# Kernel optimization log

Measured on AMD Instinct MI355X. Metric: run time of the kernel, lower is better.

## Reference

```python
import jax, jax.numpy as jnp
import numpy as np

D_MODEL, D_K, H = 1024, 64, 16
B, S = 2, 2048

def setup_inputs() -> dict:
    key = jax.random.key(0)
    ks = jax.random.split(key, 9)
    s_in = 1.0 / np.sqrt(D_MODEL)
    x = jax.random.normal(ks[0], (B, S, D_MODEL), dtype=jnp.float32)
    Wq = jax.random.uniform(ks[1], (H, D_MODEL, D_K), jnp.float32, -s_in, s_in)
    bq = jax.random.uniform(ks[2], (H, D_K), jnp.float32, -s_in, s_in)
    Wk = jax.random.uniform(ks[3], (H, D_MODEL, D_K), jnp.float32, -s_in, s_in)
    bk = jax.random.uniform(ks[4], (H, D_K), jnp.float32, -s_in, s_in)
    Wv = jax.random.uniform(ks[5], (H, D_MODEL, D_K), jnp.float32, -s_in, s_in)
    bv = jax.random.uniform(ks[6], (H, D_K), jnp.float32, -s_in, s_in)
    Wo = jax.random.uniform(ks[7], (D_MODEL, D_MODEL), jnp.float32, -s_in, s_in)
    bo = jax.random.uniform(ks[8], (D_MODEL,), jnp.float32, -s_in, s_in)
    return {"x": x, "Wq": Wq, "bq": bq, "Wk": Wk, "bk": bk,
            "Wv": Wv, "bv": bv, "Wo": Wo, "bo": bo}

def reference(x, Wq, bq, Wk, bk, Wv, bv, Wo, bo):
    # PositionLinear = Linear + ReLU (the ReLU is part of the original math)
    Q = jax.nn.relu(jnp.einsum('bsd,hdk->bhsk', x, Wq) + bq[:, None, :])
    K = jax.nn.relu(jnp.einsum('bsd,hdk->bhsk', x, Wk) + bk[:, None, :])
    V = jax.nn.relu(jnp.einsum('bsd,hdk->bhsk', x, Wv) + bv[:, None, :])
    scale = jnp.sqrt(jnp.float32(Q.shape[-1]))
    scores = jnp.einsum('bhsk,bhtk->bhst', Q, K) / scale  # [B,H,S,S]
    attn = jax.nn.softmax(scores, axis=-1)
    ctx = jnp.einsum('bhst,bhtk->bhsk', attn, V)
    # concat heads along feature dim (head order matches torch.cat(output, 2))
    ctx = jnp.transpose(ctx, (0, 2, 1, 3)).reshape(x.shape[0], x.shape[1], -1)
    out = jax.nn.relu(ctx @ Wo + bo)
    return out
```

## Files before the change

### kernel.cpp

```cpp
#include <hip/hip_runtime.h>
#include <cstddef>

#define D_MODEL 1024
#define DK 64
#define NH 16
#define NB 2
#define SEQ 2048

typedef __attribute__((ext_vector_type(8))) short bf16x8;
typedef __attribute__((ext_vector_type(4))) float floatx4;

static __device__ __forceinline__ unsigned short f2bf(float f) {
    union { float f; unsigned u; } v; v.f = f;
    unsigned r = (v.u + 0x7fffu + ((v.u >> 16) & 1u)) >> 16;
    return (unsigned short)r;
}

static __device__ __forceinline__ unsigned pk2bf(float lo, float hi) {
    unsigned ua = __float_as_uint(lo) + 0x8000u;
    unsigned ub = __float_as_uint(hi) + 0x8000u;
    return __builtin_amdgcn_perm(ub, ua, 0x07060302u);
}

static __device__ __forceinline__ float swz16(float x) {
    return __int_as_float(__builtin_amdgcn_ds_swizzle(__float_as_int(x), 0x401F));
}

static __device__ __forceinline__ void gld16(const unsigned short* g, unsigned short* l) {
    __builtin_amdgcn_global_load_lds(
        (const __attribute__((address_space(1))) unsigned int*)g,
        (__attribute__((address_space(3))) unsigned int*)l, 16, 0, 0);
}

__global__ __launch_bounds__(256) void convert_x(const float* __restrict__ x,
                                                 unsigned short* __restrict__ xb)
{
    const size_t i = ((size_t)blockIdx.x * 256 + threadIdx.x) * 16;
#pragma unroll
    for (int c = 0; c < 16; c += 4) {
        float4 v = *(const float4*)&x[i + c];
        uint2 pk;
        pk.x = (unsigned)f2bf(v.x) | ((unsigned)f2bf(v.y) << 16);
        pk.y = (unsigned)f2bf(v.z) | ((unsigned)f2bf(v.w) << 16);
        *(uint2*)&xb[i + c] = pk;
    }
}

__global__ __launch_bounds__(256) void pack_w(
    const float* __restrict__ Wq, const float* __restrict__ Wk,
    const float* __restrict__ Wv, const float* __restrict__ Wo,
    unsigned short* __restrict__ Bqkv, unsigned short* __restrict__ Bo)
{
    __shared__ float T[64][65];
    const int t   = blockIdx.x;
    const int tid = threadIdx.x;
    const int rr   = tid >> 2;
    const int cseg = (tid & 3) * 16;

    const float* src;
    unsigned short* dst;
    if (t < 768) {
        const int proj = t / 256, rem = t % 256;
        const int h = rem >> 4, d0 = (rem & 15) * 64;
        const float* W = proj == 0 ? Wq : (proj == 1 ? Wk : Wv);
        src = W + ((size_t)h * 1024 + d0) * 64;
#pragma unroll
        for (int c = 0; c < 16; c += 4) {
            float4 v = *(const float4*)&src[(size_t)rr * 64 + cseg + c];
            T[rr][cseg + c + 0] = v.x; T[rr][cseg + c + 1] = v.y;
            T[rr][cseg + c + 2] = v.z; T[rr][cseg + c + 3] = v.w;
        }
        __syncthreads();
        dst = &Bqkv[((size_t)proj * 1024 + h * 64 + rr) * 1024 + d0 + cseg];
    } else {
        const int t2 = t - 768;
        const int k0 = (t2 >> 4) * 64, nb0 = (t2 & 15) * 64;
#pragma unroll
        for (int c = 0; c < 16; c += 4) {
            float4 v = *(const float4*)&Wo[(size_t)(k0 + rr) * 1024 + nb0 + cseg + c];
            T[rr][cseg + c + 0] = v.x; T[rr][cseg + c + 1] = v.y;
            T[rr][cseg + c + 2] = v.z; T[rr][cseg + c + 3] = v.w;
        }
        __syncthreads();
        dst = &Bo[(size_t)(nb0 + rr) * 1024 + k0 + cseg];
    }
    unsigned int w[8];
#pragma unroll
    for (int ii = 0; ii < 8; ii++) {
        unsigned short lo = f2bf(T[cseg + ii * 2 + 0][rr]);
        unsigned short hi = f2bf(T[cseg + ii * 2 + 1][rr]);
        w[ii] = (unsigned)lo | ((unsigned)hi << 16);
    }
    *(uint4*)(dst + 0) = make_uint4(w[0], w[1], w[2], w[3]);
    *(uint4*)(dst + 8) = make_uint4(w[4], w[5], w[6], w[7]);
}

__global__ __launch_bounds__(256) void gemm_qkv(
    const unsigned short* __restrict__ Abf,
    const unsigned short* __restrict__ Bp,
    const float* __restrict__ bq, const float* __restrict__ bk,
    const float* __restrict__ bv,
    unsigned short* __restrict__ Qo, unsigned short* __restrict__ Ko,
    unsigned short* __restrict__ Vo)
{
    __shared__ __align__(16) unsigned short As[128 * 32];
    __shared__ __align__(16) unsigned short Bs[128 * 32];

    const int tid  = threadIdx.x;
    const int wv   = tid >> 6, lane = tid & 63;
    const int m0   = blockIdx.x * 128;
    const int n0   = blockIdx.y * 128;
    const int lq   = lane & 15, g = lane >> 4;
    const int wm   = (wv >> 1) * 64;
    const int wn   = (wv & 1) * 64;
    const int srow = lane >> 2;
    const int sseg = (lane & 3) * 8;

    floatx4 acc[4][4];
#pragma unroll
    for (int i = 0; i < 4; i++)
#pragma unroll
        for (int j = 0; j < 4; j++) acc[i][j] = (floatx4){0.f, 0.f, 0.f, 0.f};

    for (int k0 = 0; k0 < 1024; k0 += 32) {
#pragma unroll
        for (int r = 0; r < 2; r++) {
            const int chunk = wv * 2 + r;
            const int row   = chunk * 16 + srow;
            gld16(&Abf[(size_t)(m0 + row) * 1024 + k0 + sseg], &As[chunk * 512]);
            gld16(&Bp [(size_t)(n0 + row) * 1024 + k0 + sseg], &Bs[chunk * 512]);
        }
        __syncthreads();
        bf16x8 af[4], bfv[4];
#pragma unroll
        for (int i = 0; i < 4; i++)
            af[i] = *(const bf16x8*)&As[(wm + i * 16 + lq) * 32 + g * 8];
#pragma unroll
        for (int j = 0; j < 4; j++)
            bfv[j] = *(const bf16x8*)&Bs[(wn + j * 16 + lq) * 32 + g * 8];
#pragma unroll
        for (int i = 0; i < 4; i++)
#pragma unroll
            for (int j = 0; j < 4; j++)
                acc[i][j] = __builtin_amdgcn_mfma_f32_16x16x32_bf16(af[i], bfv[j], acc[i][j], 0, 0, 0);
        __syncthreads();
    }

    const int proj = n0 >> 10;
    const float* bias = proj == 0 ? bq : (proj == 1 ? bk : bv);
    unsigned short* OutQK = proj == 0 ? Qo : Ko;

#pragma unroll
    for (int j = 0; j < 4; j++) {
        const int n  = n0 + wn + j * 16 + lq;
        const int nn = n & 1023;
        const int h  = nn >> 6, dk = nn & 63;
        const float bb = bias[nn];
#pragma unroll
        for (int i = 0; i < 4; i++) {
            const int mbase = m0 + wm + i * 16 + g * 4;
            const int b_ = mbase >> 11;
            const int s_ = mbase & (SEQ - 1);
            const int bh = b_ * NH + h;
            if (proj < 2) {
                const size_t fb = (((size_t)bh * 128 + (s_ >> 4)) * 2 + (dk >> 5)) * 512
                                + (size_t)((((dk & 31) >> 3) * 16) + (s_ & 15)) * 8 + (dk & 7);
#pragma unroll
                for (int r = 0; r < 4; r++)
                    OutQK[fb + (size_t)r * 8] = f2bf(fmaxf(acc[i][j][r] + bb, 0.f));
            } else {
                const size_t fb = ((((size_t)bh * 32 + (s_ >> 6)) * 4 + (dk >> 4)) * 2
                                   + ((s_ >> 5) & 1)) * 512
                                + (size_t)((((s_ & 31) >> 3) * 16) + (dk & 15)) * 8 + (s_ & 7);
                uint2 pk;
                pk.x = (unsigned)f2bf(fmaxf(acc[i][j][0] + bb, 0.f))
                     | ((unsigned)f2bf(fmaxf(acc[i][j][1] + bb, 0.f)) << 16);
                pk.y = (unsigned)f2bf(fmaxf(acc[i][j][2] + bb, 0.f))
                     | ((unsigned)f2bf(fmaxf(acc[i][j][3] + bb, 0.f)) << 16);
                *(uint2*)&Vo[fb] = pk;
            }
        }
    }
}

__global__ __launch_bounds__(256, 2) void attn_kernel(
    const unsigned short* __restrict__ Qf,
    const unsigned short* __restrict__ Kf,
    const unsigned short* __restrict__ Vf,
    unsigned short* __restrict__ ctxb)
{
    __shared__ __align__(16) unsigned short KVs[2][8192];
    __shared__ __align__(16) unsigned short Ps[4][2][16][72];

    const int blk = blockIdx.x;
    const int xcd = blk & 7;
    const int j_  = blk >> 3;
    const int bh  = xcd * 4 + (j_ & 3);
    const int qt  = j_ >> 2;

    const int tid  = threadIdx.x;
    const int wv   = tid >> 6;
    const int lane = tid & 63;
    const int lq   = lane & 15;
    const int g    = lane >> 4;

    const int q0 = qt * 128 + wv * 32;

    const size_t qfB = ((size_t)bh * 128 + (q0 >> 4)) * 1024 + (size_t)lane * 8;
    bf16x8 q0a = *(const bf16x8*)&Qf[qfB];
    bf16x8 q0b = *(const bf16x8*)&Qf[qfB + 512];
    bf16x8 q1a = *(const bf16x8*)&Qf[qfB + 1024];
    bf16x8 q1b = *(const bf16x8*)&Qf[qfB + 1536];

    const float C  = 0.18033688011112042f;
    const float MC = 2.8853900817779267f;

    const unsigned short* KtB = &Kf[(size_t)bh * 131072];
    const unsigned short* VtB = &Vf[(size_t)bh * 131072];

    float l0 = 0.f, l1 = 0.f;
    floatx4 acc0[4], acc1[4];
#pragma unroll
    for (int i = 0; i < 4; i++) {
        acc0[i] = (floatx4){0.f, 0.f, 0.f, 0.f};
        acc1[i] = (floatx4){0.f, 0.f, 0.f, 0.f};
    }

#pragma unroll
    for (int r = 0; r < 2; r++) {
        const int c = wv * 2 + r;
        gld16(&KtB[(size_t)c * 512 + lane * 8], &KVs[0][c * 512]);
        gld16(&VtB[(size_t)c * 512 + lane * 8], &KVs[0][4096 + c * 512]);
    }
    __syncthreads();

    for (int jt = 0; jt < SEQ / 64; jt++) {
        const int buf = jt & 1;

        const int jn = (jt + 1) & (SEQ / 64 - 1);
        const unsigned short* ktn = &KtB[(size_t)jn * 4096];
        const unsigned short* vtn = &VtB[(size_t)jn * 4096];
#pragma unroll
        for (int r = 0; r < 2; r++) {
            const int c = wv * 2 + r;
            gld16(&ktn[(size_t)c * 512 + lane * 8], &KVs[buf ^ 1][c * 512]);
            gld16(&vtn[(size_t)c * 512 + lane * 8], &KVs[buf ^ 1][4096 + c * 512]);
        }

        const unsigned short* kb = &KVs[buf][0];
        const unsigned short* vb = &KVs[buf][4096];

        floatx4 s0[4], s1[4];
#pragma unroll
        for (int mt = 0; mt < 4; mt++) {
            bf16x8 a0 = *(const bf16x8*)&kb[mt * 1024 + lane * 8];
            bf16x8 a1 = *(const bf16x8*)&kb[mt * 1024 + 512 + lane * 8];
            s0[mt] = (floatx4){0.f, 0.f, 0.f, 0.f};
            s0[mt] = __builtin_amdgcn_mfma_f32_16x16x32_bf16(a0, q0a, s0[mt], 0, 0, 0);
            s0[mt] = __builtin_amdgcn_mfma_f32_16x16x32_bf16(a1, q0b, s0[mt], 0, 0, 0);
            s1[mt] = (floatx4){0.f, 0.f, 0.f, 0.f};
            s1[mt] = __builtin_amdgcn_mfma_f32_16x16x32_bf16(a0, q1a, s1[mt], 0, 0, 0);
            s1[mt] = __builtin_amdgcn_mfma_f32_16x16x32_bf16(a1, q1b, s1[mt], 0, 0, 0);
        }

        bf16x8 vr[8];
#pragma unroll
        for (int nt = 0; nt < 4; nt++) {
            vr[nt]     = *(const bf16x8*)&vb[nt * 1024 + lane * 8];
            vr[4 + nt] = *(const bf16x8*)&vb[nt * 1024 + 512 + lane * 8];
        }

#pragma unroll
        for (int mt = 0; mt < 4; mt++) {
            float p00 = __builtin_amdgcn_exp2f(fmaf(s0[mt][0], C, -MC));
            float p01 = __builtin_amdgcn_exp2f(fmaf(s0[mt][1], C, -MC));
            float p02 = __builtin_amdgcn_exp2f(fmaf(s0[mt][2], C, -MC));
            float p03 = __builtin_amdgcn_exp2f(fmaf(s0[mt][3], C, -MC));
            l0 += (p00 + p01) + (p02 + p03);
            uint2 pk;
            pk.x = pk2bf(p00, p01);
            pk.y = pk2bf(p02, p03);
            *(uint2*)&Ps[wv][0][lq][mt * 16 + g * 4] = pk;
            float p10 = __builtin_amdgcn_exp2f(fmaf(s1[mt][0], C, -MC));
            float p11 = __builtin_amdgcn_exp2f(fmaf(s1[mt][1], C, -MC));
            float p12 = __builtin_amdgcn_exp2f(fmaf(s1[mt][2], C, -MC));
            float p13 = __builtin_amdgcn_exp2f(fmaf(s1[mt][3], C, -MC));
            l1 += (p10 + p11) + (p12 + p13);
            uint2 pk1;
            pk1.x = pk2bf(p10, p11);
            pk1.y = pk2bf(p12, p13);
            *(uint2*)&Ps[wv][1][lq][mt * 16 + g * 4] = pk1;
        }
        __builtin_amdgcn_s_waitcnt(0xC07F);
        bf16x8 pb00 = *(const bf16x8*)&Ps[wv][0][lq][g * 8];
        bf16x8 pb01 = *(const bf16x8*)&Ps[wv][0][lq][32 + g * 8];
        bf16x8 pb10 = *(const bf16x8*)&Ps[wv][1][lq][g * 8];
        bf16x8 pb11 = *(const bf16x8*)&Ps[wv][1][lq][32 + g * 8];

#pragma unroll
        for (int nt = 0; nt < 4; nt++) {
            acc0[nt] = __builtin_amdgcn_mfma_f32_16x16x32_bf16(vr[nt],     pb00, acc0[nt], 0, 0, 0);
            acc0[nt] = __builtin_amdgcn_mfma_f32_16x16x32_bf16(vr[4 + nt], pb01, acc0[nt], 0, 0, 0);
            acc1[nt] = __builtin_amdgcn_mfma_f32_16x16x32_bf16(vr[nt],     pb10, acc1[nt], 0, 0, 0);
            acc1[nt] = __builtin_amdgcn_mfma_f32_16x16x32_bf16(vr[4 + nt], pb11, acc1[nt], 0, 0, 0);
        }

        __syncthreads();
    }

    l0 += swz16(l0); l0 += __shfl_xor(l0, 32, 64);
    l1 += swz16(l1); l1 += __shfl_xor(l1, 32, 64);
    const float li0 = 1.f / l0, li1 = 1.f / l1;
    const int b_ = bh >> 4, h_ = bh & 15;
#pragma unroll
    for (int nt = 0; nt < 4; nt++) {
        uint2 pk;
        pk.x = pk2bf(acc0[nt][0] * li0, acc0[nt][1] * li0);
        pk.y = pk2bf(acc0[nt][2] * li0, acc0[nt][3] * li0);
        *(uint2*)&ctxb[((size_t)(b_ * SEQ) + q0 + lq) * D_MODEL + h_ * DK + nt * 16 + g * 4] = pk;
        uint2 pk1;
        pk1.x = pk2bf(acc1[nt][0] * li1, acc1[nt][1] * li1);
        pk1.y = pk2bf(acc1[nt][2] * li1, acc1[nt][3] * li1);
        *(uint2*)&ctxb[((size_t)(b_ * SEQ) + q0 + 16 + lq) * D_MODEL + h_ * DK + nt * 16 + g * 4] = pk1;
    }
}

__global__ __launch_bounds__(256) void gemm_o(
    const unsigned short* __restrict__ Abf,
    const unsigned short* __restrict__ Bp,
    const float* __restrict__ bo,
    float* __restrict__ out)
{
    __shared__ __align__(16) unsigned short As[128 * 32];
    __shared__ __align__(16) unsigned short Bs[128 * 32];

    const int tid  = threadIdx.x;
    const int wv   = tid >> 6, lane = tid & 63;
    const int m0   = blockIdx.x * 128;
    const int n0   = blockIdx.y * 128;
    const int lq   = lane & 15, g = lane >> 4;
    const int wm   = (wv >> 1) * 64;
    const int wn   = (wv & 1) * 64;
    const int srow = lane >> 2;
    const int sseg = (lane & 3) * 8;

    floatx4 acc[4][4];
#pragma unroll
    for (int i = 0; i < 4; i++)
#pragma unroll
        for (int j = 0; j < 4; j++) acc[i][j] = (floatx4){0.f, 0.f, 0.f, 0.f};

    for (int k0 = 0; k0 < 1024; k0 += 32) {
#pragma unroll
        for (int r = 0; r < 2; r++) {
            const int chunk = wv * 2 + r;
            const int row   = chunk * 16 + srow;
            gld16(&Abf[(size_t)(m0 + row) * 1024 + k0 + sseg], &As[chunk * 512]);
            gld16(&Bp [(size_t)(n0 + row) * 1024 + k0 + sseg], &Bs[chunk * 512]);
        }
        __syncthreads();
        bf16x8 af[4], bfv[4];
#pragma unroll
        for (int i = 0; i < 4; i++)
            af[i] = *(const bf16x8*)&As[(wm + i * 16 + lq) * 32 + g * 8];
#pragma unroll
        for (int j = 0; j < 4; j++)
            bfv[j] = *(const bf16x8*)&Bs[(wn + j * 16 + lq) * 32 + g * 8];
#pragma unroll
        for (int i = 0; i < 4; i++)
#pragma unroll
            for (int j = 0; j < 4; j++)
                acc[i][j] = __builtin_amdgcn_mfma_f32_16x16x32_bf16(af[i], bfv[j], acc[i][j], 0, 0, 0);
        __syncthreads();
    }

#pragma unroll
    for (int j = 0; j < 4; j++) {
        const int n  = n0 + wn + j * 16 + lq;
        const float bb = bo[n];
#pragma unroll
        for (int i = 0; i < 4; i++) {
#pragma unroll
            for (int r = 0; r < 4; r++) {
                const int m = m0 + wm + i * 16 + g * 4 + r;
                out[(size_t)m * 1024 + n] = fmaxf(acc[i][j][r] + bb, 0.f);
            }
        }
    }
}

extern "C" void kernel_launch(void* const* d_in, const int* in_sizes, int n_in,
                              void* d_out, int out_size, void* d_ws, size_t ws_size,
                              hipStream_t stream) {
    const float* x  = (const float*)d_in[0];
    const float* Wq = (const float*)d_in[1];
    const float* bq = (const float*)d_in[2];
    const float* Wk = (const float*)d_in[3];
    const float* bk = (const float*)d_in[4];
    const float* Wv = (const float*)d_in[5];
    const float* bv = (const float*)d_in[6];
    const float* Wo = (const float*)d_in[7];
    const float* bo = (const float*)d_in[8];
    float* out = (float*)d_out;

    const size_t perE = (size_t)NB * NH * SEQ * DK;
    unsigned short* xbf  = (unsigned short*)d_ws;
    unsigned short* Bqkv = xbf  + (size_t)4096 * 1024;
    unsigned short* Bo   = Bqkv + (size_t)3072 * 1024;
    unsigned short* Qfr  = Bo   + (size_t)1024 * 1024;
    unsigned short* Kfr  = Qfr + perE;
    unsigned short* Vfr  = Kfr + perE;
    unsigned short* Cbf  = Vfr + perE;

    convert_x<<<1024, 256, 0, stream>>>(x, xbf);
    pack_w<<<1024, 256, 0, stream>>>(Wq, Wk, Wv, Wo, Bqkv, Bo);
    gemm_qkv<<<dim3(32, 24), 256, 0, stream>>>(xbf, Bqkv, bq, bk, bv, Qfr, Kfr, Vfr);
    attn_kernel<<<512, 256, 0, stream>>>(Qfr, Kfr, Vfr, Cbf);
    gemm_o<<<dim3(32, 8), 256, 0, stream>>>(Cbf, Bo, bo, out);
}
```

Baseline: 196.4 us.

## Split attention work across waves by key halves with LDS reduction

```diff
diff --git a/kernel.cpp b/kernel.cpp
--- a/kernel.cpp
+++ b/kernel.cpp
@@ -190,7 +190,8 @@
     unsigned short* __restrict__ ctxb)
 {
     __shared__ __align__(16) unsigned short KVs[2][8192];
-    __shared__ __align__(16) unsigned short Ps[4][2][16][72];
+    __shared__ __align__(16) unsigned short Ps[4][4][16][40];
+    __shared__ float Lx[2][4][64];
 
     const int blk = blockIdx.x;
     const int xcd = blk & 7;
@@ -203,14 +204,18 @@
     const int lane = tid & 63;
     const int lq   = lane & 15;
     const int g    = lane >> 4;
-
-    const int q0 = qt * 128 + wv * 32;
-
+    const int qh   = wv >> 1;
+    const int kh   = wv & 1;
+
+    const int q0 = qt * 128 + qh * 64;
+
+    bf16x8 qa[4], qb[4];
     const size_t qfB = ((size_t)bh * 128 + (q0 >> 4)) * 1024 + (size_t)lane * 8;
-    bf16x8 q0a = *(const bf16x8*)&Qf[qfB];
-    bf16x8 q0b = *(const bf16x8*)&Qf[qfB + 512];
-    bf16x8 q1a = *(const bf16x8*)&Qf[qfB + 1024];
-    bf16x8 q1b = *(const bf16x8*)&Qf[qfB + 1536];
+#pragma unroll
+    for (int t = 0; t < 4; t++) {
+        qa[t] = *(const bf16x8*)&Qf[qfB + (size_t)t * 1024];
+        qb[t] = *(const bf16x8*)&Qf[qfB + (size_t)t * 1024 + 512];
+    }
 
     const float C  = 0.18033688011112042f;
     const float MC = 2.8853900817779267f;
@@ -218,13 +223,12 @@
     const unsigned short* KtB = &Kf[(size_t)bh * 131072];
     const unsigned short* VtB = &Vf[(size_t)bh * 131072];
 
-    float l0 = 0.f, l1 = 0.f;
-    floatx4 acc0[4], acc1[4];
-#pragma unroll
-    for (int i = 0; i < 4; i++) {
-        acc0[i] = (floatx4){0.f, 0.f, 0.f, 0.f};
-        acc1[i] = (floatx4){0.f, 0.f, 0.f, 0.f};
-    }
+    float l[4] = {0.f, 0.f, 0.f, 0.f};
+    floatx4 acc[4][4];
+#pragma unroll
+    for (int t = 0; t < 4; t++)
+#pragma unroll
+        for (int n = 0; n < 4; n++) acc[t][n] = (floatx4){0.f, 0.f, 0.f, 0.f};
 
 #pragma unroll
     for (int r = 0; r < 2; r++) {
@@ -250,78 +254,95 @@
         const unsigned short* kb = &KVs[buf][0];
         const unsigned short* vb = &KVs[buf][4096];
 
-        floatx4 s0[4], s1[4];
-#pragma unroll
-        for (int mt = 0; mt < 4; mt++) {
-            bf16x8 a0 = *(const bf16x8*)&kb[mt * 1024 + lane * 8];
-            bf16x8 a1 = *(const bf16x8*)&kb[mt * 1024 + 512 + lane * 8];
-            s0[mt] = (floatx4){0.f, 0.f, 0.f, 0.f};
-            s0[mt] = __builtin_amdgcn_mfma_f32_16x16x32_bf16(a0, q0a, s0[mt], 0, 0, 0);
-            s0[mt] = __builtin_amdgcn_mfma_f32_16x16x32_bf16(a1, q0b, s0[mt], 0, 0, 0);
-            s1[mt] = (floatx4){0.f, 0.f, 0.f, 0.f};
-            s1[mt] = __builtin_amdgcn_mfma_f32_16x16x32_bf16(a0, q1a, s1[mt], 0, 0, 0);
-            s1[mt] = __builtin_amdgcn_mfma_f32_16x16x32_bf16(a1, q1b, s1[mt], 0, 0, 0);
-        }
-
-        bf16x8 vr[8];
-#pragma unroll
-        for (int nt = 0; nt < 4; nt++) {
-            vr[nt]     = *(const bf16x8*)&vb[nt * 1024 + lane * 8];
-            vr[4 + nt] = *(const bf16x8*)&vb[nt * 1024 + 512 + lane * 8];
-        }
-
-#pragma unroll
-        for (int mt = 0; mt < 4; mt++) {
-            float p00 = __builtin_amdgcn_exp2f(fmaf(s0[mt][0], C, -MC));
-            float p01 = __builtin_amdgcn_exp2f(fmaf(s0[mt][1], C, -MC));
-            float p02 = __builtin_amdgcn_exp2f(fmaf(s0[mt][2], C, -MC));
-            float p03 = __builtin_amdgcn_exp2f(fmaf(s0[mt][3], C, -MC));
-            l0 += (p00 + p01) + (p02 + p03);
-            uint2 pk;
-            pk.x = pk2bf(p00, p01);
-            pk.y = pk2bf(p02, p03);
-            *(uint2*)&Ps[wv][0][lq][mt * 16 + g * 4] = pk;
-            float p10 = __builtin_amdgcn_exp2f(fmaf(s1[mt][0], C, -MC));
-            float p11 = __builtin_amdgcn_exp2f(fmaf(s1[mt][1], C, -MC));
-            float p12 = __builtin_amdgcn_exp2f(fmaf(s1[mt][2], C, -MC));
-            float p13 = __builtin_amdgcn_exp2f(fmaf(s1[mt][3], C, -MC));
-            l1 += (p10 + p11) + (p12 + p13);
+        bf16x8 k0a = *(const bf16x8*)&kb[(2 * kh + 0) * 1024 + lane * 8];
+        bf16x8 k0b = *(const bf16x8*)&kb[(2 * kh + 0) * 1024 + 512 + lane * 8];
+        bf16x8 k1a = *(const bf16x8*)&kb[(2 * kh + 1) * 1024 + lane * 8];
+        bf16x8 k1b = *(const bf16x8*)&kb[(2 * kh + 1) * 1024 + 512 + lane * 8];
+
+        bf16x8 vr[4];
+#pragma unroll
+        for (int n = 0; n < 4; n++)
+            vr[n] = *(const bf16x8*)&vb[(n * 2 + kh) * 512 + lane * 8];
+
+#pragma unroll
+        for (int t = 0; t < 4; t++) {
+            floatx4 s0 = (floatx4){0.f, 0.f, 0.f, 0.f};
+            s0 = __builtin_amdgcn_mfma_f32_16x16x32_bf16(k0a, qa[t], s0, 0, 0, 0);
+            s0 = __builtin_amdgcn_mfma_f32_16x16x32_bf16(k0b, qb[t], s0, 0, 0, 0);
+            floatx4 s1 = (floatx4){0.f, 0.f, 0.f, 0.f};
+            s1 = __builtin_amdgcn_mfma_f32_16x16x32_bf16(k1a, qa[t], s1, 0, 0, 0);
+            s1 = __builtin_amdgcn_mfma_f32_16x16x32_bf16(k1b, qb[t], s1, 0, 0, 0);
+
+            float p00 = __builtin_amdgcn_exp2f(fmaf(s0[0], C, -MC));
+            float p01 = __builtin_amdgcn_exp2f(fmaf(s0[1], C, -MC));
+            float p02 = __builtin_amdgcn_exp2f(fmaf(s0[2], C, -MC));
+            float p03 = __builtin_amdgcn_exp2f(fmaf(s0[3], C, -MC));
+            l[t] += (p00 + p01) + (p02 + p03);
+            uint2 pk0;
+            pk0.x = pk2bf(p00, p01);
+            pk0.y = pk2bf(p02, p03);
+            *(uint2*)&Ps[wv][t][lq][g * 4] = pk0;
+
+            float p10 = __builtin_amdgcn_exp2f(fmaf(s1[0], C, -MC));
+            float p11 = __builtin_amdgcn_exp2f(fmaf(s1[1], C, -MC));
+            float p12 = __builtin_amdgcn_exp2f(fmaf(s1[2], C, -MC));
+            float p13 = __builtin_amdgcn_exp2f(fmaf(s1[3], C, -MC));
+            l[t] += (p10 + p11) + (p12 + p13);
             uint2 pk1;
             pk1.x = pk2bf(p10, p11);
             pk1.y = pk2bf(p12, p13);
-            *(uint2*)&Ps[wv][1][lq][mt * 16 + g * 4] = pk1;
+            *(uint2*)&Ps[wv][t][lq][16 + g * 4] = pk1;
         }
         __builtin_amdgcn_s_waitcnt(0xC07F);
-        bf16x8 pb00 = *(const bf16x8*)&Ps[wv][0][lq][g * 8];
-        bf16x8 pb01 = *(const bf16x8*)&Ps[wv][0][lq][32 + g * 8];
-        bf16x8 pb10 = *(const bf16x8*)&Ps[wv][1][lq][g * 8];
-        bf16x8 pb11 = *(const bf16x8*)&Ps[wv][1][lq][32 + g * 8];
-
-#pragma unroll
-        for (int nt = 0; nt < 4; nt++) {
-            acc0[nt] = __builtin_amdgcn_mfma_f32_16x16x32_bf16(vr[nt],     pb00, acc0[nt], 0, 0, 0);
-            acc0[nt] = __builtin_amdgcn_mfma_f32_16x16x32_bf16(vr[4 + nt], pb01, acc0[nt], 0, 0, 0);
-            acc1[nt] = __builtin_amdgcn_mfma_f32_16x16x32_bf16(vr[nt],     pb10, acc1[nt], 0, 0, 0);
-            acc1[nt] = __builtin_amdgcn_mfma_f32_16x16x32_bf16(vr[4 + nt], pb11, acc1[nt], 0, 0, 0);
-        }
-
-        __syncthreads();
-    }
-
-    l0 += swz16(l0); l0 += __shfl_xor(l0, 32, 64);
-    l1 += swz16(l1); l1 += __shfl_xor(l1, 32, 64);
-    const float li0 = 1.f / l0, li1 = 1.f / l1;
-    const int b_ = bh >> 4, h_ = bh & 15;
-#pragma unroll
-    for (int nt = 0; nt < 4; nt++) {
-        uint2 pk;
-        pk.x = pk2bf(acc0[nt][0] * li0, acc0[nt][1] * li0);
-        pk.y = pk2bf(acc0[nt][2] * li0, acc0[nt][3] * li0);
-        *(uint2*)&ctxb[((size_t)(b_ * SEQ) + q0 + lq) * D_MODEL + h_ * DK + nt * 16 + g * 4] = pk;
-        uint2 pk1;
-        pk1.x = pk2bf(acc1[nt][0] * li1, acc1[nt][1] * li1);
-        pk1.y = pk2bf(acc1[nt][2] * li1, acc1[nt][3] * li1);
-        *(uint2*)&ctxb[((size_t)(b_ * SEQ) + q0 + 16 + lq) * D_MODEL + h_ * DK + nt * 16 + g * 4] = pk1;
+
+        bf16x8 pb[4];
+#pragma unroll
+        for (int t = 0; t < 4; t++)
+            pb[t] = *(const bf16x8*)&Ps[wv][t][lq][g * 8];
+
+#pragma unroll
+        for (int t = 0; t < 4; t++)
+#pragma unroll
+            for (int n = 0; n < 4; n++)
+                acc[t][n] = __builtin_amdgcn_mfma_f32_16x16x32_bf16(vr[n], pb[t], acc[t][n], 0, 0, 0);
+
+        __syncthreads();
+    }
+
+#pragma unroll
+    for (int t = 0; t < 4; t++) {
+        l[t] += swz16(l[t]);
+        l[t] += __shfl_xor(l[t], 32, 64);
+    }
+
+    float* red = (float*)&KVs[0][0] + (size_t)qh * 4096;
+    if (kh == 1) {
+#pragma unroll
+        for (int t = 0; t < 4; t++) {
+#pragma unroll
+            for (int n = 0; n < 4; n++)
+                *(floatx4*)&red[(t * 4 + n) * 256 + lane * 4] = acc[t][n];
+            Lx[qh][t][lane] = l[t];
+        }
+    }
+    __syncthreads();
+    if (kh == 0) {
+        const int b_ = bh >> 4, h_ = bh & 15;
+#pragma unroll
+        for (int t = 0; t < 4; t++) {
+            const float lt = l[t] + Lx[qh][t][lane];
+            const float li = 1.f / lt;
+#pragma unroll
+            for (int n = 0; n < 4; n++) {
+                floatx4 a = acc[t][n];
+                floatx4 b = *(const floatx4*)&red[(t * 4 + n) * 256 + lane * 4];
+                uint2 pk;
+                pk.x = pk2bf((a[0] + b[0]) * li, (a[1] + b[1]) * li);
+                pk.y = pk2bf((a[2] + b[2]) * li, (a[3] + b[3]) * li);
+                *(uint2*)&ctxb[((size_t)(b_ * SEQ) + q0 + t * 16 + lq) * D_MODEL
+                               + h_ * DK + n * 16 + g * 4] = pk;
+            }
+        }
     }
 }
 
```

New measurement: 193.5 us. About the same (-1.5%).
